# Performance work log

Measured on AMD Instinct MI355X. Metric: run time of the kernel, lower is better.

Reference implementation:

```python
import jax, jax.numpy as jnp
import numpy as np

BATCH, SEQ, IN, HID, OUT = 64, 512, 512, 1024, 512


def setup_inputs() -> dict:
    key = jax.random.key(0)
    ks = jax.random.split(key, 7)
    s_ih = 1.0 / np.sqrt(IN)
    s_hh = 1.0 / np.sqrt(HID)
    return {
        "x_sequence": jax.random.normal(ks[0], (BATCH, SEQ, IN), dtype=jnp.float32),
        "W_ih": jax.random.uniform(ks[1], (HID, IN), jnp.float32, -s_ih, s_ih),
        "b_ih": jax.random.uniform(ks[2], (HID,), jnp.float32, -s_ih, s_ih),
        "W_hh": jax.random.uniform(ks[3], (HID, HID), jnp.float32, -s_hh, s_hh),
        "b_hh": jax.random.uniform(ks[4], (HID,), jnp.float32, -s_hh, s_hh),
        "W_ho": jax.random.uniform(ks[5], (OUT, HID), jnp.float32, -s_hh, s_hh),
        "b_ho": jax.random.uniform(ks[6], (OUT,), jnp.float32, -s_hh, s_hh),
    }


def reference(x_sequence, W_ih, b_ih, W_hh, b_hh, W_ho, b_ho):
    # Elman RNN: h_t = tanh(x_t @ W_ih^T + b_ih + h_{t-1} @ W_hh^T + b_hh)
    # Returned output is the projection of the FINAL hidden state only
    # (per-step outputs in the original are detached bookkeeping).
    # Precompute all input projections in one big GEMM: [B,S,H]
    x_proj = jnp.einsum("bsi,hi->bsh", x_sequence, W_ih) + b_ih + b_hh

    def step(h, xp_t):
        h_new = jnp.tanh(xp_t + h @ W_hh.T)
        return h_new, None

    h0 = jnp.zeros((x_sequence.shape[0], W_hh.shape[0]), dtype=x_sequence.dtype)
    h_final, _ = jax.lax.scan(step, h0, jnp.swapaxes(x_proj, 0, 1))  # scan over time
    output = h_final @ W_ho.T + b_ho  # [B, OUT]
    return output
```

## Files before the change

kernel.cpp:

```cpp
#include <hip/hip_runtime.h>
#include <cstdint>
#include <cstddef>

typedef unsigned short ushort_t;
typedef unsigned int uint_t;
typedef unsigned long long u64_t;
typedef __attribute__((ext_vector_type(8))) short frag16;
typedef __attribute__((ext_vector_type(8))) unsigned short u16x8;
typedef __attribute__((ext_vector_type(4))) float f32x4;

#define SEQ   512
#define INF   512
#define HID   1024
#define OUTF  512
#define GROUPS 16
#define BPG    16
#define NB     4
#define RPB    64
#define SPIN_LIMIT (1 << 18)

__device__ __forceinline__ float b2f(ushort_t u) {
    union { unsigned int i; float f; } v; v.i = ((unsigned int)u) << 16; return v.f;
}
__device__ __forceinline__ ushort_t f2b(float f) {
    unsigned int u = __float_as_uint(f);
    unsigned int r = (u + 0x7fffu + ((u >> 16) & 1u)) >> 16;
    return (ushort_t)r;
}
__device__ __forceinline__ float fast_tanh(float s) {
    const float e = __expf(2.0f * s);
    return 1.0f - 2.0f * __builtin_amdgcn_rcpf(e + 1.0f);
}

__device__ __forceinline__ void cvt8_hilo(const float* __restrict__ src, u16x8* hi, u16x8* lo) {
    const float4 x0 = *(const float4*)src;
    const float4 x1 = *(const float4*)(src + 4);
    float xs[8] = {x0.x,x0.y,x0.z,x0.w,x1.x,x1.y,x1.z,x1.w};
    u16x8 h, l;
#pragma unroll
    for (int j = 0; j < 8; ++j) {
        const ushort_t hb = f2b(xs[j]);
        h[j] = hb;
        l[j] = f2b(xs[j] - b2f(hb));
    }
    *hi = h; if (lo) *lo = l;
}
__device__ __forceinline__ u16x8 cvt8_hi(const float* __restrict__ src) {
    const float4 x0 = *(const float4*)src;
    const float4 x1 = *(const float4*)(src + 4);
    float xs[8] = {x0.x,x0.y,x0.z,x0.w,x1.x,x1.y,x1.z,x1.w};
    u16x8 h;
#pragma unroll
    for (int j = 0; j < 8; ++j) h[j] = f2b(xs[j]);
    return h;
}

__global__ __launch_bounds__(256, 2)
void xproj_kernel(const float* __restrict__ X, const float* __restrict__ Wih,
                  const float* __restrict__ bih, const float* __restrict__ bhh,
                  float* __restrict__ XP)
{
    __shared__ ushort_t Ah[128][40];
    __shared__ ushort_t Al[128][40];
    __shared__ ushort_t Bs[128][40];
    const int tid = (int)threadIdx.x;
    const int m0 = (int)blockIdx.x * 128;
    const int n0 = (int)blockIdx.y * 128;
    const int w  = tid >> 6, l = tid & 63;
    const int wm = (w & 1) * 64, wn = (w >> 1) * 64;
    const int lm = l & 15, lg = l >> 4, hk = lg * 8;
    const int sr = tid >> 2, sc = (tid & 3) * 8;

    f32x4 acc[4][4];
#pragma unroll
    for (int a = 0; a < 4; ++a)
#pragma unroll
        for (int b = 0; b < 4; ++b) { acc[a][b][0]=0.f; acc[a][b][1]=0.f; acc[a][b][2]=0.f; acc[a][b][3]=0.f; }

    for (int ko = 0; ko < INF; ko += 32) {
        __syncthreads();
        u16x8 h, lo;
        cvt8_hilo(&X[(size_t)(m0+sr)*INF + ko + sc], &h, &lo);
        *(u16x8*)&Ah[sr][sc] = h;  *(u16x8*)&Al[sr][sc] = lo;
        cvt8_hilo(&X[(size_t)(m0+sr+64)*INF + ko + sc], &h, &lo);
        *(u16x8*)&Ah[sr+64][sc] = h;  *(u16x8*)&Al[sr+64][sc] = lo;
        *(u16x8*)&Bs[sr][sc]    = cvt8_hi(&Wih[(size_t)(n0+sr)*INF + ko + sc]);
        *(u16x8*)&Bs[sr+64][sc] = cvt8_hi(&Wih[(size_t)(n0+sr+64)*INF + ko + sc]);
        __syncthreads();
        frag16 afh[4], afl[4], bf[4];
#pragma unroll
        for (int i = 0; i < 4; ++i) afh[i] = *(const frag16*)&Ah[wm + i*16 + lm][hk];
#pragma unroll
        for (int i = 0; i < 4; ++i) afl[i] = *(const frag16*)&Al[wm + i*16 + lm][hk];
#pragma unroll
        for (int i = 0; i < 4; ++i) bf[i]  = *(const frag16*)&Bs[wn + i*16 + lm][hk];
#pragma unroll
        for (int a = 0; a < 4; ++a)
#pragma unroll
            for (int b = 0; b < 4; ++b) {
                acc[a][b] = __builtin_amdgcn_mfma_f32_16x16x32_bf16(afh[a], bf[b], acc[a][b], 0, 0, 0);
                acc[a][b] = __builtin_amdgcn_mfma_f32_16x16x32_bf16(afl[a], bf[b], acc[a][b], 0, 0, 0);
            }
    }

#pragma unroll
    for (int b = 0; b < 4; ++b) {
        const int n = n0 + wn + b*16 + lm;
        const float bias = bih[n] + bhh[n];
#pragma unroll
        for (int a = 0; a < 4; ++a)
#pragma unroll
            for (int q = 0; q < 4; ++q) {
                const int m = m0 + wm + a*16 + lg*4 + q;
                XP[(size_t)m * HID + n] = acc[a][b][q] + bias;
            }
    }
}

__global__ __launch_bounds__(256, 1)
void rnn_scan_kernel(const float* __restrict__ XP, const float* __restrict__ Whh,
                     u64_t* __restrict__ Hbuf)
{
    __shared__ ushort_t Ws[RPB][1032];
    __shared__ uint_t   Hst[NB][1028];
    __shared__ float    Cred[4][4][4][16];

    const int tid = (int)threadIdx.x;
    const int w = tid >> 6, l = tid & 63;
    const int lm = l & 15, lg = l >> 4;
    const int gid = (int)blockIdx.x >> 4;
    const int r   = (int)blockIdx.x & 15;
    const int b0 = gid * NB;
    const int j0 = r * RPB;

    {
        const int rr = tid >> 2, cq = (tid & 3) * 256;
        const float* src = Whh + (size_t)(j0 + rr) * HID + cq;
#pragma unroll
        for (int i = 0; i < 32; ++i)
            *(u16x8*)&Ws[rr][cq + i*8] = cvt8_hi(&src[i*8]);
    }
    __syncthreads();

    for (int t = 0; t < SEQ; ++t) {
        float xpv[4];
        if (l < 16) {
#pragma unroll
            for (int q = 0; q < 4; ++q)
                xpv[q] = XP[(size_t)((b0 + q) * SEQ + t) * HID + (j0 + w*16 + l)];
        }

        if (t > 0) {
            {
                const u64_t* rowp = Hbuf + ((size_t)((t - 1) & 1) * 64 + b0 + w) * 1024 + l;
                const uint_t want = (uint_t)t;
                u64_t v[16];
#pragma unroll
                for (int j = 0; j < 16; ++j)
                    v[j] = __hip_atomic_load(&rowp[j*64], __ATOMIC_RELAXED,
                                             __HIP_MEMORY_SCOPE_AGENT);
                int spin = 0;
                for (;;) {
                    int bad = 0;
#pragma unroll
                    for (int j = 0; j < 16; ++j) bad |= ((uint_t)v[j] != want);
                    if (!__any(bad)) break;
                    if (++spin > SPIN_LIMIT) break;
                    __builtin_amdgcn_s_sleep(1);
#pragma unroll
                    for (int j = 0; j < 16; ++j)
                        if ((uint_t)v[j] != want)
                            v[j] = __hip_atomic_load(&rowp[j*64], __ATOMIC_RELAXED,
                                                     __HIP_MEMORY_SCOPE_AGENT);
                }
#pragma unroll
                for (int j = 0; j < 16; ++j)
                    Hst[w][l + 64*j] = (uint_t)(v[j] >> 32);
            }
            __syncthreads();

            f32x4 acc[4];
#pragma unroll
            for (int i = 0; i < 4; ++i) { acc[i][0]=0.f; acc[i][1]=0.f; acc[i][2]=0.f; acc[i][3]=0.f; }
            const int kbase = w * 256;
#pragma unroll
            for (int kk = 0; kk < 256; kk += 32) {
                const int k0 = kbase + kk;
                frag16 ahi, alo;
#pragma unroll
                for (int j = 0; j < 8; ++j) { ahi[j] = 0; alo[j] = 0; }
                if (lm < NB) {
                    const uint_t* hr = &Hst[lm][k0 + lg*8];
                    const uint4 d0 = *(const uint4*)hr;
                    const uint4 d1 = *(const uint4*)(hr + 4);
                    uint_t dd[8] = {d0.x,d0.y,d0.z,d0.w,d1.x,d1.y,d1.z,d1.w};
#pragma unroll
                    for (int j = 0; j < 8; ++j) {
                        ahi[j] = (short)(dd[j] & 0xffffu);
                        alo[j] = (short)(dd[j] >> 16);
                    }
                }
#pragma unroll
                for (int tl = 0; tl < 4; ++tl) {
                    const frag16 wf = *(const frag16*)&Ws[tl*16 + lm][k0 + lg*8];
                    acc[tl] = __builtin_amdgcn_mfma_f32_16x16x32_bf16(ahi, wf, acc[tl], 0, 0, 0);
                    acc[tl] = __builtin_amdgcn_mfma_f32_16x16x32_bf16(alo, wf, acc[tl], 0, 0, 0);
                }
            }
            if (lg == 0) {
#pragma unroll
                for (int tl = 0; tl < 4; ++tl)
#pragma unroll
                    for (int q = 0; q < 4; ++q)
                        Cred[w][tl][q][lm] = acc[tl][q];
            }
            __syncthreads();
        }

        if (l < 16) {
            const int jt = j0 + w*16 + l;
            u64_t* outp = Hbuf + ((size_t)(t & 1) * 64 + b0) * 1024 + jt;
#pragma unroll
            for (int q = 0; q < 4; ++q) {
                float s = 0.f;
                if (t > 0)
                    s = Cred[0][w][q][l] + Cred[1][w][q][l]
                      + Cred[2][w][q][l] + Cred[3][w][q][l];
                const float v = fast_tanh(s + xpv[q]);
                const ushort_t hi = f2b(v);
                const ushort_t lo = f2b(v - b2f(hi));
                const u64_t pk = ((u64_t)((uint_t)hi | ((uint_t)lo << 16)) << 32)
                               | (u64_t)(uint_t)(t + 1);
                __hip_atomic_store(&outp[(size_t)q * 1024], pk,
                                   __ATOMIC_RELAXED, __HIP_MEMORY_SCOPE_AGENT);
            }
        }
    }
}

__global__ __launch_bounds__(256)
void outproj_kernel(const u64_t* __restrict__ Hp, const float* __restrict__ Who,
                    const float* __restrict__ bho, float* __restrict__ Out)
{
    const int tid = (int)threadIdx.x;
    const int w = tid >> 6, l = tid & 63;
    const int lm = l & 15, lg = l >> 4, hk = lg * 8;
    const int n0 = (int)blockIdx.x * 64;

    f32x4 acc[4];
#pragma unroll
    for (int i = 0; i < 4; ++i) { acc[i][0]=0.f; acc[i][1]=0.f; acc[i][2]=0.f; acc[i][3]=0.f; }

    for (int k0 = 0; k0 < HID; k0 += 32) {
        const u64_t* hr = Hp + (size_t)(w*16 + lm) * HID + k0 + hk;
        frag16 ahi, alo;
#pragma unroll
        for (int j = 0; j < 8; ++j) {
            const uint_t d = (uint_t)(hr[j] >> 32);
            ahi[j] = (short)(d & 0xffffu);
            alo[j] = (short)(d >> 16);
        }
#pragma unroll
        for (int bi = 0; bi < 4; ++bi) {
            const u16x8 bv = cvt8_hi(&Who[(size_t)(n0 + bi*16 + lm) * HID + k0 + hk]);
            acc[bi] = __builtin_amdgcn_mfma_f32_16x16x32_bf16(ahi, (frag16)bv, acc[bi], 0, 0, 0);
            acc[bi] = __builtin_amdgcn_mfma_f32_16x16x32_bf16(alo, (frag16)bv, acc[bi], 0, 0, 0);
        }
    }
#pragma unroll
    for (int bi = 0; bi < 4; ++bi) {
        const int n = n0 + bi*16 + lm;
        const float bias = bho[n];
#pragma unroll
        for (int q = 0; q < 4; ++q) {
            const int b = w*16 + lg*4 + q;
            Out[(size_t)b * OUTF + n] = acc[bi][q] + bias;
        }
    }
}

extern "C" void kernel_launch(void* const* d_in, const int* in_sizes, int n_in,
                              void* d_out, int out_size, void* d_ws, size_t ws_size,
                              hipStream_t stream)
{
    const float* X   = (const float*)d_in[0];
    const float* Wih = (const float*)d_in[1];
    const float* bih = (const float*)d_in[2];
    const float* Whh = (const float*)d_in[3];
    const float* bhh = (const float*)d_in[4];
    const float* Who = (const float*)d_in[5];
    const float* bho = (const float*)d_in[6];
    float* Out = (float*)d_out;

    char* ws = (char*)d_ws;
    float* XP = (float*)ws;
    u64_t* Hbuf = (u64_t*)(ws + (size_t)32768 * 1024 * 4);

    xproj_kernel<<<dim3(256, 8), dim3(256), 0, stream>>>(X, Wih, bih, bhh, XP);

    rnn_scan_kernel<<<dim3(GROUPS * BPG), dim3(256), 0, stream>>>(XP, Whh, Hbuf);

    outproj_kernel<<<dim3(OUTF / 64), dim3(256), 0, stream>>>(Hbuf + (size_t)64 * 1024,
                                                              Who, bho, Out);
}
```

Before: 2.108 ms.

## Prefetch next-step hidden state and inputs, split hi/lo LDS planes, lighter barriers

The recurrent scan loop is reorganised. The first step is peeled out. The next step's hidden-state loads and XP values are issued before the current step's results are stored, so their global latency overlaps the publish. Hidden state in LDS is split into separate hi and lo bf16 planes, which removes per-fragment unpacking and the lm<NB branch. The Ws stride is padded to 1040. __syncthreads is replaced by a custom lgkmcnt-only barrier. The early loads may read stale flags and fall into the spin loop, and the custom barrier relies on there being no outstanding global-memory ordering needs.

```diff
diff --git a/kernel.cpp b/kernel.cpp
--- a/kernel.cpp
+++ b/kernel.cpp
@@ -17,6 +17,7 @@
 #define BPG    16
 #define NB     4
 #define RPB    64
+#define WSTR   1040
 #define SPIN_LIMIT (1 << 18)
 
 __device__ __forceinline__ float b2f(ushort_t u) {
@@ -30,6 +31,13 @@
 __device__ __forceinline__ float fast_tanh(float s) {
     const float e = __expf(2.0f * s);
     return 1.0f - 2.0f * __builtin_amdgcn_rcpf(e + 1.0f);
+}
+
+__device__ __forceinline__ void lds_barrier() {
+    asm volatile("s_waitcnt lgkmcnt(0)" ::: "memory");
+    __builtin_amdgcn_sched_barrier(0);
+    __builtin_amdgcn_s_barrier();
+    __builtin_amdgcn_sched_barrier(0);
 }
 
 __device__ __forceinline__ void cvt8_hilo(const float* __restrict__ src, u16x8* hi, u16x8* lo) {
@@ -121,8 +129,9 @@
 void rnn_scan_kernel(const float* __restrict__ XP, const float* __restrict__ Whh,
                      u64_t* __restrict__ Hbuf)
 {
-    __shared__ ushort_t Ws[RPB][1032];
-    __shared__ uint_t   Hst[NB][1028];
+    __shared__ ushort_t Ws[RPB][WSTR];
+    __shared__ ushort_t Hhi[NB][WSTR];
+    __shared__ ushort_t Hlo[NB][WSTR];
     __shared__ float    Cred[4][4][4][16];
 
     const int tid = (int)threadIdx.x;
@@ -140,100 +149,136 @@
         for (int i = 0; i < 32; ++i)
             *(u16x8*)&Ws[rr][cq + i*8] = cvt8_hi(&src[i*8]);
     }
-    __syncthreads();
-
-    for (int t = 0; t < SEQ; ++t) {
-        float xpv[4];
-        if (l < 16) {
+    lds_barrier();
+
+    float xpv[4];
+    if (lg == 0) {
+#pragma unroll
+        for (int q = 0; q < 4; ++q)
+            xpv[q] = XP[(size_t)((b0 + q) * SEQ + 0) * HID + (j0 + w*16 + lm)];
+    }
+
+    u64_t v[16];
+
+    {
+        u64_t pk[4];
+        if (lg == 0) {
+#pragma unroll
+            for (int q = 0; q < 4; ++q) {
+                const float hv = fast_tanh(xpv[q]);
+                const ushort_t hi = f2b(hv);
+                const ushort_t lo = f2b(hv - b2f(hi));
+                pk[q] = ((u64_t)((uint_t)hi | ((uint_t)lo << 16)) << 32) | 1ull;
+            }
+        }
+        {
+            const u64_t* rown = Hbuf + ((size_t)0 * 64 + b0 + w) * 1024 + l;
+#pragma unroll
+            for (int j = 0; j < 16; ++j)
+                v[j] = __hip_atomic_load(&rown[j*64], __ATOMIC_RELAXED,
+                                         __HIP_MEMORY_SCOPE_AGENT);
+        }
+        if (lg == 0) {
 #pragma unroll
             for (int q = 0; q < 4; ++q)
-                xpv[q] = XP[(size_t)((b0 + q) * SEQ + t) * HID + (j0 + w*16 + l)];
-        }
-
-        if (t > 0) {
-            {
-                const u64_t* rowp = Hbuf + ((size_t)((t - 1) & 1) * 64 + b0 + w) * 1024 + l;
-                const uint_t want = (uint_t)t;
-                u64_t v[16];
+                xpv[q] = XP[(size_t)((b0 + q) * SEQ + 1) * HID + (j0 + w*16 + lm)];
+        }
+        if (lg == 0) {
+            u64_t* outp = Hbuf + ((size_t)0 * 64 + b0) * 1024 + (j0 + w*16 + lm);
+#pragma unroll
+            for (int q = 0; q < 4; ++q)
+                __hip_atomic_store(&outp[(size_t)q * 1024], pk[q],
+                                   __ATOMIC_RELAXED, __HIP_MEMORY_SCOPE_AGENT);
+        }
+    }
+
+    for (int t = 1; t < SEQ; ++t) {
+        {
+            const u64_t* rowp = Hbuf + ((size_t)((t - 1) & 1) * 64 + b0 + w) * 1024 + l;
+            const uint_t want = (uint_t)t;
+            int spin = 0;
+            for (;;) {
+                int bad = 0;
+#pragma unroll
+                for (int j = 0; j < 16; ++j) bad |= ((uint_t)v[j] != want);
+                if (!__any(bad)) break;
+                if (++spin > SPIN_LIMIT) break;
+                __builtin_amdgcn_s_sleep(1);
 #pragma unroll
                 for (int j = 0; j < 16; ++j)
-                    v[j] = __hip_atomic_load(&rowp[j*64], __ATOMIC_RELAXED,
-                                             __HIP_MEMORY_SCOPE_AGENT);
-                int spin = 0;
-                for (;;) {
-                    int bad = 0;
-#pragma unroll
-                    for (int j = 0; j < 16; ++j) bad |= ((uint_t)v[j] != want);
-                    if (!__any(bad)) break;
-                    if (++spin > SPIN_LIMIT) break;
-                    __builtin_amdgcn_s_sleep(1);
-#pragma unroll
-                    for (int j = 0; j < 16; ++j)
-                        if ((uint_t)v[j] != want)
-                            v[j] = __hip_atomic_load(&rowp[j*64], __ATOMIC_RELAXED,
-                                                     __HIP_MEMORY_SCOPE_AGENT);
-                }
-#pragma unroll
-                for (int j = 0; j < 16; ++j)
-                    Hst[w][l + 64*j] = (uint_t)(v[j] >> 32);
-            }
-            __syncthreads();
-
-            f32x4 acc[4];
-#pragma unroll
-            for (int i = 0; i < 4; ++i) { acc[i][0]=0.f; acc[i][1]=0.f; acc[i][2]=0.f; acc[i][3]=0.f; }
-            const int kbase = w * 256;
+                    if ((uint_t)v[j] != want)
+                        v[j] = __hip_atomic_load(&rowp[j*64], __ATOMIC_RELAXED,
+                                                 __HIP_MEMORY_SCOPE_AGENT);
+            }
+        }
+#pragma unroll
+        for (int j = 0; j < 16; ++j) {
+            const uint_t d = (uint_t)(v[j] >> 32);
+            Hhi[w][l + 64*j] = (ushort_t)(d & 0xffffu);
+            Hlo[w][l + 64*j] = (ushort_t)(d >> 16);
+        }
+        lds_barrier();
+
+        f32x4 acc[4];
+#pragma unroll
+        for (int i = 0; i < 4; ++i) { acc[i][0]=0.f; acc[i][1]=0.f; acc[i][2]=0.f; acc[i][3]=0.f; }
+        {
+            const int kbase = w * 256 + lg * 8;
+            const ushort_t* ph = &Hhi[lm & 3][kbase];
+            const ushort_t* pl = &Hlo[lm & 3][kbase];
+            const ushort_t* pw = &Ws[lm][kbase];
 #pragma unroll
             for (int kk = 0; kk < 256; kk += 32) {
-                const int k0 = kbase + kk;
-                frag16 ahi, alo;
-#pragma unroll
-                for (int j = 0; j < 8; ++j) { ahi[j] = 0; alo[j] = 0; }
-                if (lm < NB) {
-                    const uint_t* hr = &Hst[lm][k0 + lg*8];
-                    const uint4 d0 = *(const uint4*)hr;
-                    const uint4 d1 = *(const uint4*)(hr + 4);
-                    uint_t dd[8] = {d0.x,d0.y,d0.z,d0.w,d1.x,d1.y,d1.z,d1.w};
-#pragma unroll
-                    for (int j = 0; j < 8; ++j) {
-                        ahi[j] = (short)(dd[j] & 0xffffu);
-                        alo[j] = (short)(dd[j] >> 16);
-                    }
-                }
+                const frag16 ahi = *(const frag16*)(ph + kk);
+                const frag16 alo = *(const frag16*)(pl + kk);
 #pragma unroll
                 for (int tl = 0; tl < 4; ++tl) {
-                    const frag16 wf = *(const frag16*)&Ws[tl*16 + lm][k0 + lg*8];
+                    const frag16 wf = *(const frag16*)(pw + (size_t)tl * 16 * WSTR + kk);
                     acc[tl] = __builtin_amdgcn_mfma_f32_16x16x32_bf16(ahi, wf, acc[tl], 0, 0, 0);
                     acc[tl] = __builtin_amdgcn_mfma_f32_16x16x32_bf16(alo, wf, acc[tl], 0, 0, 0);
                 }
             }
+        }
+        if (lg == 0) {
+#pragma unroll
+            for (int tl = 0; tl < 4; ++tl)
+#pragma unroll
+                for (int q = 0; q < 4; ++q)
+                    Cred[w][tl][q][lm] = acc[tl][q];
+        }
+        lds_barrier();
+
+        u64_t pk[4];
+        if (lg == 0) {
+#pragma unroll
+            for (int q = 0; q < 4; ++q) {
+                const float s = (Cred[0][w][q][lm] + Cred[1][w][q][lm])
+                              + (Cred[2][w][q][lm] + Cred[3][w][q][lm]);
+                const float hv = fast_tanh(s + xpv[q]);
+                const ushort_t hi = f2b(hv);
+                const ushort_t lo = f2b(hv - b2f(hi));
+                pk[q] = ((u64_t)((uint_t)hi | ((uint_t)lo << 16)) << 32)
+                      | (u64_t)(uint_t)(t + 1);
+            }
+        }
+        if (t + 1 < SEQ) {
+            const u64_t* rown = Hbuf + ((size_t)(t & 1) * 64 + b0 + w) * 1024 + l;
+#pragma unroll
+            for (int j = 0; j < 16; ++j)
+                v[j] = __hip_atomic_load(&rown[j*64], __ATOMIC_RELAXED,
+                                         __HIP_MEMORY_SCOPE_AGENT);
             if (lg == 0) {
 #pragma unroll
-                for (int tl = 0; tl < 4; ++tl)
-#pragma unroll
-                    for (int q = 0; q < 4; ++q)
-                        Cred[w][tl][q][lm] = acc[tl][q];
-            }
-            __syncthreads();
-        }
-
-        if (l < 16) {
-            const int jt = j0 + w*16 + l;
-            u64_t* outp = Hbuf + ((size_t)(t & 1) * 64 + b0) * 1024 + jt;
-#pragma unroll
-            for (int q = 0; q < 4; ++q) {
-                float s = 0.f;
-                if (t > 0)
-                    s = Cred[0][w][q][l] + Cred[1][w][q][l]
-                      + Cred[2][w][q][l] + Cred[3][w][q][l];
-                const float v = fast_tanh(s + xpv[q]);
-                const ushort_t hi = f2b(v);
-                const ushort_t lo = f2b(v - b2f(hi));
-                const u64_t pk = ((u64_t)((uint_t)hi | ((uint_t)lo << 16)) << 32)
-                               | (u64_t)(uint_t)(t + 1);
-                __hip_atomic_store(&outp[(size_t)q * 1024], pk,
+                for (int q = 0; q < 4; ++q)
+                    xpv[q] = XP[(size_t)((b0 + q) * SEQ + (t + 1)) * HID + (j0 + w*16 + lm)];
+            }
+        }
+        if (lg == 0) {
+            u64_t* outp = Hbuf + ((size_t)(t & 1) * 64 + b0) * 1024 + (j0 + w*16 + lm);
+#pragma unroll
+            for (int q = 0; q < 4; ++q)
+                __hip_atomic_store(&outp[(size_t)q * 1024], pk[q],
                                    __ATOMIC_RELAXED, __HIP_MEMORY_SCOPE_AGENT);
-            }
         }
     }
 }
```

Result: no change. 2.129 ms (+1.0%).
